# Optimization experiments

Hardware: AMD Instinct MI355X
Metric: run time of the kernel (lower is better)

The kernel has to match this reference:

```python
import jax, jax.numpy as jnp
import numpy as np

B, L, D = 2, 2048, 1024
H, DK, DV = 16, 64, 64
EPS = 1e-6


def setup_inputs() -> dict:
    key = jax.random.key(0)
    ks = jax.random.split(key, 7)
    s = 0.02
    return {
        "x": jax.random.normal(ks[0], (B, L, D), dtype=jnp.float32),
        "Wq": jax.random.normal(ks[1], (D, H * DK), dtype=jnp.float32) * s,
        "Wk": jax.random.normal(ks[2], (D, H * DK), dtype=jnp.float32) * s,
        "Wv": jax.random.normal(ks[3], (D, H * DV), dtype=jnp.float32) * s,
        "Wo": jax.random.normal(ks[4], (H * DV, D), dtype=jnp.float32) * s,
        "ln_gamma": jnp.ones((D,), dtype=jnp.float32),
        "ln_beta": jnp.zeros((D,), dtype=jnp.float32),
    }


def reference(x, Wq, Wk, Wv, Wo, ln_gamma, ln_beta):
    temp = jnp.asarray(DK, x.dtype) ** 0.5
    # projections -> [B, H, L, Dh]
    q = (x @ Wq).reshape(B, L, H, DK).transpose(0, 2, 1, 3)
    k = (x @ Wk).reshape(B, L, H, DK).transpose(0, 2, 1, 3)
    v = (x @ Wv).reshape(B, L, H, DV).transpose(0, 2, 1, 3)
    # naive attention: explicit [B,H,L,L] scores (dropout rate 0 -> identity)
    scores = jnp.einsum("bhqd,bhkd->bhqk", q / temp, k)
    attn = jax.nn.softmax(scores, axis=-1)
    o = jnp.einsum("bhqk,bhkd->bhqd", attn, v)
    o = o.transpose(0, 2, 1, 3).reshape(B, L, H * DV)
    out = o @ Wo + x  # residual
    # LayerNorm(eps=1e-6)
    mu = jnp.mean(out, axis=-1, keepdims=True)
    var = jnp.var(out, axis=-1, keepdims=True)
    return (out - mu) * jax.lax.rsqrt(var + EPS) * ln_gamma + ln_beta
```

## Files before the change

kernel.cpp:

```cpp
#include <hip/hip_runtime.h>


typedef __bf16 bf16;
typedef __bf16 bf16x2 __attribute__((ext_vector_type(2)));
typedef __bf16 bf16x4 __attribute__((ext_vector_type(4)));
typedef __bf16 bf16x8 __attribute__((ext_vector_type(8)));
typedef float floatx4 __attribute__((ext_vector_type(4)));
typedef int intx4 __attribute__((ext_vector_type(4)));

#define MFMA16(a, b, c) __builtin_amdgcn_mfma_f32_16x16x32_bf16((a), (b), (c), 0, 0, 0)

__device__ __forceinline__ void gll16(const bf16* g, bf16* l) {
  __builtin_amdgcn_global_load_lds((const __attribute__((address_space(1))) void*)g,
                                   (__attribute__((address_space(3))) void*)l, 16, 0, 0);
}

__global__ __launch_bounds__(256) void k_prep_x(const float* __restrict__ x, bf16* __restrict__ xb) {
  const int i = (blockIdx.x * 256 + threadIdx.x) * 4;
  const float4 v = *reinterpret_cast<const float4*>(x + i);
  bf16x4 o = {(bf16)v.x, (bf16)v.y, (bf16)v.z, (bf16)v.w};
  *reinterpret_cast<bf16x4*>(xb + i) = o;
}

__global__ __launch_bounds__(256) void k_prep_w(const float* __restrict__ Wq, const float* __restrict__ Wk,
                                                const float* __restrict__ Wv, const float* __restrict__ Wo,
                                                bf16* __restrict__ WT) {
  __shared__ float tile[32][33];
  const int z = blockIdx.z;
  const float* W = (z == 0) ? Wq : (z == 1) ? Wk : (z == 2) ? Wv : Wo;
  const int n0 = blockIdx.x * 32, k0 = blockIdx.y * 32;
  const int tx = threadIdx.x, ty = threadIdx.y;
#pragma unroll
  for (int j = 0; j < 32; j += 8)
    tile[ty + j][tx] = W[(size_t)(k0 + ty + j) * 1024 + n0 + tx];
  __syncthreads();
#pragma unroll
  for (int j = 0; j < 32; j += 8)
    WT[(size_t)(z * 1024 + n0 + ty + j) * 1024 + k0 + tx] = (bf16)tile[tx][ty + j];
}

template <int MODE>
__global__ __launch_bounds__(256) void k_gemm(const bf16* __restrict__ A, const bf16* __restrict__ Bt,
                                              const float* __restrict__ X, float* __restrict__ Y,
                                              bf16* __restrict__ QB, bf16* __restrict__ KB,
                                              bf16* __restrict__ VTB) {
  __shared__ __align__(16) bf16 As[3 * 128 * 64];
  __shared__ __align__(16) bf16 Bs[3 * 128 * 64];
  const int t = threadIdx.x;
  const int lane = t & 63, wv = t >> 6;
  const int qd = lane >> 4, col = lane & 15;
  const int c7 = col & 7;
  const int wm = wv >> 1, wn = wv & 1;
  const int m0 = blockIdx.x * 128, n0 = blockIdx.y * 128;
  const int srow = wv * 8 + (lane >> 3);
  const int scol = ((lane & 7) ^ (lane >> 3)) * 8;
  const bf16* Ag = A + (size_t)(m0 + srow) * 1024 + scol;
  const bf16* Bg = Bt + (size_t)(n0 + srow) * 1024 + scol;

  floatx4 acc[4][4] = {};

#define GSTAGE(bu, ti)                                                                              \
  do {                                                                                              \
    _Pragma("unroll") for (int rd = 0; rd < 4; rd++) {                                              \
      gll16(Ag + (size_t)rd * 32 * 1024 + (ti) * 64, As + (bu) * 8192 + (rd * 32 + wv * 8) * 64);   \
      gll16(Bg + (size_t)rd * 32 * 1024 + (ti) * 64, Bs + (bu) * 8192 + (rd * 32 + wv * 8) * 64);   \
    }                                                                                               \
  } while (0)

#define GCOMP(bu)                                                                                   \
  do {                                                                                              \
    const bf16* as_ = As + (bu) * 8192;                                                             \
    const bf16* bs_ = Bs + (bu) * 8192;                                                             \
    _Pragma("unroll") for (int ks = 0; ks < 2; ks++) {                                              \
      bf16x8 af[4], bfr[4];                                                                         \
      _Pragma("unroll") for (int i = 0; i < 4; i++)                                                 \
        af[i] = *reinterpret_cast<const bf16x8*>(as_ + (wm * 64 + i * 16 + col) * 64 +              \
                                                 ((ks * 4 + qd) ^ c7) * 8);                         \
      _Pragma("unroll") for (int i = 0; i < 4; i++)                                                 \
        bfr[i] = *reinterpret_cast<const bf16x8*>(bs_ + (wn * 64 + i * 16 + col) * 64 +             \
                                                  ((ks * 4 + qd) ^ c7) * 8);                        \
      _Pragma("unroll") for (int i = 0; i < 4; i++)                                                 \
        _Pragma("unroll") for (int j = 0; j < 4; j++)                                               \
          acc[i][j] = MFMA16(af[i], bfr[j], acc[i][j]);                                             \
    }                                                                                               \
  } while (0)

#define GITER(cur, prv, ti)                                            \
  do {                                                                 \
    asm volatile("s_waitcnt vmcnt(8)" ::: "memory");                   \
    __builtin_amdgcn_s_barrier();                                      \
    GCOMP(cur);                                                        \
    __builtin_amdgcn_s_barrier();                                      \
    GSTAGE(prv, ((ti) + 2 <= 15) ? ((ti) + 2) : 15);                   \
  } while (0)

  GSTAGE(0, 0);
  GSTAGE(1, 1);
  asm volatile("s_waitcnt vmcnt(8)" ::: "memory");
  __builtin_amdgcn_s_barrier();
  GCOMP(0);
  __builtin_amdgcn_s_barrier();
  GSTAGE(2, 2);
  for (int j = 1; j < 16; j += 3) {
    GITER(1, 0, j);
    GITER(2, 1, j + 1);
    GITER(0, 2, j + 2);
  }
#undef GSTAGE
#undef GCOMP
#undef GITER

#pragma unroll
  for (int i = 0; i < 4; i++) {
#pragma unroll
    for (int j = 0; j < 4; j++) {
      const int mb = m0 + wm * 64 + i * 16 + qd * 4;
      const int n = n0 + wn * 64 + j * 16 + col;
      if (MODE == 0) {
        const int seg = n >> 10;
        const int h = (n & 1023) >> 6, dd = n & 63;
#pragma unroll
        for (int r = 0; r < 4; r++) {
          const int m = mb + r;
          const int bb = m >> 11, l = m & 2047;
          const float v = acc[i][j][r];
          if (seg == 0)
            QB[((size_t)(bb * 16 + h) * 2048 + l) * 64 + dd] = (bf16)(v * 0.18033688f);
          else if (seg == 1)
            KB[((size_t)(bb * 16 + h) * 2048 + l) * 64 + dd] = (bf16)v;
          else
            VTB[((size_t)(bb * 16 + h) * 64 + dd) * 2048 + l] = (bf16)v;
        }
      } else {
#pragma unroll
        for (int r = 0; r < 4; r++) {
          const int m = mb + r;
          Y[(size_t)m * 1024 + n] = acc[i][j][r] + X[(size_t)m * 1024 + n];
        }
      }
    }
  }
}

__global__ __launch_bounds__(256) void k_attn(const bf16* __restrict__ QB, const bf16* __restrict__ KB,
                                              const bf16* __restrict__ VTB, bf16* __restrict__ OB) {
  __shared__ __align__(16) bf16 Ks[3][64 * 64];
  __shared__ __align__(16) bf16 Vs[3][64 * 64];
  const int t = threadIdx.x;
  const int lane = t & 63, wv = t >> 6;
  const int qd = lane >> 4, col = lane & 15;
  const int c7 = col & 7;
  const int bh = blockIdx.y;
  const int qr = blockIdx.x * 128 + wv * 32;
  const int lrow0 = wv * 8 + (lane >> 3);
  const int scol = ((lane & 7) ^ (lane >> 3)) * 8;
  const int kg0 = ((lrow0 >> 5) << 5) + (((lrow0 >> 2) & 3) << 3) + (((lrow0 >> 4) & 1) << 2) + (lrow0 & 3);
  const int r1 = lrow0 + 32;
  const int kg1 = ((r1 >> 5) << 5) + (((r1 >> 2) & 3) << 3) + (((r1 >> 4) & 1) << 2) + (r1 & 3);
  const bf16* Kg0 = KB + ((size_t)bh * 2048 + kg0) * 64 + scol;
  const bf16* Kg1 = KB + ((size_t)bh * 2048 + kg1) * 64 + scol;
  const bf16* Vg0 = VTB + ((size_t)bh * 64 + lrow0) * 2048 + scol;
  const bf16* Vg1 = VTB + ((size_t)bh * 64 + lrow0 + 32) * 2048 + scol;

  bf16x8 bQ[2][2];
#pragma unroll
  for (int qt = 0; qt < 2; qt++)
#pragma unroll
    for (int s = 0; s < 2; s++)
      bQ[qt][s] = *reinterpret_cast<const bf16x8*>(QB + ((size_t)bh * 2048 + qr + qt * 16 + col) * 64 + s * 32 + qd * 8);

  floatx4 oacc[2][4] = {};
  float lsum[2] = {0.f, 0.f};
  floatx4 scur[2][4];
  int pk[2][4][2];

#define STAGE(bu, ti)                                                  \
  do {                                                                 \
    gll16(Kg0 + (size_t)(ti) * 4096, &Ks[bu][(wv * 8) * 64]);          \
    gll16(Kg1 + (size_t)(ti) * 4096, &Ks[bu][(32 + wv * 8) * 64]);     \
    gll16(Vg0 + (ti) * 64, &Vs[bu][(wv * 8) * 64]);                    \
    gll16(Vg1 + (ti) * 64, &Vs[bu][(32 + wv * 8) * 64]);               \
  } while (0)

#define QK(bu)                                                                                      \
  do {                                                                                              \
    const bf16* ks_ = Ks[bu];                                                                       \
    _Pragma("unroll") for (int nt = 0; nt < 4; nt++) {                                              \
      bf16x8 a0 = *reinterpret_cast<const bf16x8*>(ks_ + (nt * 16 + col) * 64 + (qd ^ c7) * 8);     \
      bf16x8 a1 = *reinterpret_cast<const bf16x8*>(ks_ + (nt * 16 + col) * 64 + ((4 + qd) ^ c7) * 8); \
      _Pragma("unroll") for (int qt = 0; qt < 2; qt++) {                                            \
        floatx4 zz = {0.f, 0.f, 0.f, 0.f};                                                          \
        zz = MFMA16(a0, bQ[qt][0], zz);                                                             \
        zz = MFMA16(a1, bQ[qt][1], zz);                                                             \
        scur[qt][nt] = zz;                                                                          \
      }                                                                                             \
    }                                                                                               \
  } while (0)

#define EXPPACK()                                                                               \
  do {                                                                                          \
    _Pragma("unroll") for (int qt = 0; qt < 2; qt++) {                                          \
      _Pragma("unroll") for (int nt = 0; nt < 4; nt++) {                                        \
        const float e0 = __builtin_amdgcn_exp2f(scur[qt][nt][0]);                               \
        const float e1 = __builtin_amdgcn_exp2f(scur[qt][nt][1]);                               \
        const float e2 = __builtin_amdgcn_exp2f(scur[qt][nt][2]);                               \
        const float e3 = __builtin_amdgcn_exp2f(scur[qt][nt][3]);                               \
        lsum[qt] += (e0 + e1) + (e2 + e3);                                                      \
        bf16x2 p01, p23;                                                                        \
        p01[0] = (bf16)e0; p01[1] = (bf16)e1;                                                   \
        p23[0] = (bf16)e2; p23[1] = (bf16)e3;                                                   \
        pk[qt][nt][0] = __builtin_bit_cast(int, p01);                                           \
        pk[qt][nt][1] = __builtin_bit_cast(int, p23);                                           \
      }                                                                                         \
    }                                                                                           \
  } while (0)

#define PV(bu)                                                                                      \
  do {                                                                                              \
    const bf16* vs_ = Vs[bu];                                                                       \
    bf16x8 bV[4][2];                                                                                \
    _Pragma("unroll") for (int nd = 0; nd < 4; nd++) {                                              \
      bV[nd][0] = *reinterpret_cast<const bf16x8*>(vs_ + (nd * 16 + col) * 64 + (qd ^ c7) * 8);     \
      bV[nd][1] = *reinterpret_cast<const bf16x8*>(vs_ + (nd * 16 + col) * 64 + ((4 + qd) ^ c7) * 8); \
    }                                                                                               \
    _Pragma("unroll") for (int qt = 0; qt < 2; qt++) {                                              \
      _Pragma("unroll") for (int s = 0; s < 2; s++) {                                               \
        intx4 w;                                                                                    \
        w[0] = pk[qt][2 * s][0]; w[1] = pk[qt][2 * s][1];                                           \
        w[2] = pk[qt][2 * s + 1][0]; w[3] = pk[qt][2 * s + 1][1];                                   \
        const bf16x8 aP = __builtin_bit_cast(bf16x8, w);                                            \
        _Pragma("unroll") for (int nd = 0; nd < 4; nd++)                                            \
          oacc[qt][nd] = MFMA16(aP, bV[nd][s], oacc[qt][nd]);                                       \
      }                                                                                             \
    }                                                                                               \
  } while (0)

#define ITER(cur, prv, ti)                                             \
  do {                                                                 \
    asm volatile("s_waitcnt vmcnt(4)" ::: "memory");                   \
    __builtin_amdgcn_s_barrier();                                      \
    EXPPACK();                                                         \
    QK(cur);                                                           \
    PV(prv);                                                           \
    __builtin_amdgcn_s_barrier();                                      \
    STAGE(prv, ((ti) + 2 <= 31) ? ((ti) + 2) : 31);                    \
  } while (0)

  STAGE(0, 0);
  STAGE(1, 1);
  asm volatile("s_waitcnt vmcnt(4)" ::: "memory");
  __builtin_amdgcn_s_barrier();
  QK(0);
  __builtin_amdgcn_s_barrier();
  STAGE(2, 2);
  for (int j = 1; j < 30; j += 3) {
    ITER(1, 0, j);
    ITER(2, 1, j + 1);
    ITER(0, 2, j + 2);
  }
  ITER(1, 0, 31);
  EXPPACK();
  PV(1);

#pragma unroll
  for (int qt = 0; qt < 2; qt++) {
    lsum[qt] += __shfl_xor(lsum[qt], 16);
    lsum[qt] += __shfl_xor(lsum[qt], 32);
  }
  const int bb = bh >> 4, h = bh & 15;
#pragma unroll
  for (int qt = 0; qt < 2; qt++) {
#pragma unroll
    for (int r = 0; r < 4; r++) {
      const float linv = 1.f / __shfl(lsum[qt], qd * 4 + r);
      const size_t m = (size_t)bb * 2048 + qr + qt * 16 + qd * 4 + r;
#pragma unroll
      for (int nd = 0; nd < 4; nd++)
        OB[m * 1024 + h * 64 + nd * 16 + col] = (bf16)(oacc[qt][nd][r] * linv);
    }
  }
#undef STAGE
#undef QK
#undef EXPPACK
#undef PV
#undef ITER
}

__global__ __launch_bounds__(256) void k_ln(const float* __restrict__ Yin, const float* __restrict__ gamma,
                                            const float* __restrict__ beta, float* __restrict__ out) {
  __shared__ float red[8];
  const int row = blockIdx.x, t = threadIdx.x;
  const float4 v = *reinterpret_cast<const float4*>(Yin + (size_t)row * 1024 + t * 4);
  float s = v.x + v.y + v.z + v.w;
  float ss = v.x * v.x + v.y * v.y + v.z * v.z + v.w * v.w;
#pragma unroll
  for (int d = 1; d < 64; d <<= 1) {
    s += __shfl_xor(s, d);
    ss += __shfl_xor(ss, d);
  }
  if ((t & 63) == 0) {
    red[t >> 6] = s;
    red[4 + (t >> 6)] = ss;
  }
  __syncthreads();
  s = red[0] + red[1] + red[2] + red[3];
  ss = red[4] + red[5] + red[6] + red[7];
  const float mu = s * (1.f / 1024.f);
  const float var = ss * (1.f / 1024.f) - mu * mu;
  const float rs = rsqrtf(var + 1e-6f);
  const float4 g = *reinterpret_cast<const float4*>(gamma + t * 4);
  const float4 bt = *reinterpret_cast<const float4*>(beta + t * 4);
  float4 o;
  o.x = (v.x - mu) * rs * g.x + bt.x;
  o.y = (v.y - mu) * rs * g.y + bt.y;
  o.z = (v.z - mu) * rs * g.z + bt.z;
  o.w = (v.w - mu) * rs * g.w + bt.w;
  *reinterpret_cast<float4*>(out + (size_t)row * 1024 + t * 4) = o;
}

extern "C" void kernel_launch(void* const* d_in, const int* in_sizes, int n_in,
                              void* d_out, int out_size, void* d_ws, size_t ws_size,
                              hipStream_t stream) {
  (void)in_sizes; (void)n_in; (void)out_size; (void)ws_size;
  const float* x = (const float*)d_in[0];
  const float* Wq = (const float*)d_in[1];
  const float* Wk = (const float*)d_in[2];
  const float* Wv = (const float*)d_in[3];
  const float* Wo = (const float*)d_in[4];
  const float* gamma = (const float*)d_in[5];
  const float* beta = (const float*)d_in[6];

  char* ws = (char*)d_ws;
  const size_t MB = 1ull << 20;
  bf16* XB = (bf16*)(ws);
  bf16* OB = (bf16*)(ws);
  bf16* WT = (bf16*)(ws + 8 * MB);
  bf16* QB = (bf16*)(ws + 16 * MB);
  bf16* KB = (bf16*)(ws + 24 * MB);
  bf16* VTB = (bf16*)(ws + 32 * MB);
  float* Y = (float*)(ws + 16 * MB);

  k_prep_x<<<4096, 256, 0, stream>>>(x, XB);
  k_prep_w<<<dim3(32, 32, 4), dim3(32, 8), 0, stream>>>(Wq, Wk, Wv, Wo, WT);
  k_gemm<0><<<dim3(32, 24), 256, 0, stream>>>(XB, WT, nullptr, nullptr, QB, KB, VTB);
  k_attn<<<dim3(16, 32), 256, 0, stream>>>(QB, KB, VTB, OB);
  k_gemm<1><<<dim3(32, 8), 256, 0, stream>>>(OB, WT + (size_t)3072 * 1024, x, Y,
                                             nullptr, nullptr, nullptr);
  k_ln<<<4096, 256, 0, stream>>>(Y, gamma, beta, (float*)d_out);
}
```

Before: 210.1 us.

## Use 256x256 tiled QKV GEMM and double-buffer the generic GEMM

Adds a new 512-thread QKV projection kernel with 256x256 output tiles, each wave computing 128x64, and a double-buffered async LDS pipeline. The larger tile raises arithmetic intensity and cuts global reloads of A and B. The trade is 192 blocks on a large GPU, which means lower occupancy and under one wave of blocks per CU. The output-projection GEMM also moves from a triple-buffered pipeline with partial vmcnt waits to double buffering with full vmcnt(0) waits and __syncthreads. That exposes more memory latency in that kernel.

```diff
diff --git a/kernel.cpp b/kernel.cpp
--- a/kernel.cpp
+++ b/kernel.cpp
@@ -39,13 +39,104 @@
     WT[(size_t)(z * 1024 + n0 + ty + j) * 1024 + k0 + tx] = (bf16)tile[tx][ty + j];
 }
 
+__global__ __launch_bounds__(512) void k_gemm256(const bf16* __restrict__ A, const bf16* __restrict__ Bt,
+                                                 bf16* __restrict__ QB, bf16* __restrict__ KB,
+                                                 bf16* __restrict__ VTB) {
+  __shared__ __align__(16) bf16 As[2 * 256 * 64];
+  __shared__ __align__(16) bf16 Bs[2 * 256 * 64];
+  const int t = threadIdx.x;
+  const int lane = t & 63, wv = t >> 6;
+  const int qd = lane >> 4, col = lane & 15;
+  const int c7 = col & 7;
+  const int wm = wv >> 2, wn = wv & 3;
+  const int m0 = blockIdx.x * 256, n0 = blockIdx.y * 256;
+  const int srow = wv * 8 + (lane >> 3);
+  const int scol = ((lane & 7) ^ (lane >> 3)) * 8;
+  const bf16* Ag = A + (size_t)(m0 + srow) * 1024 + scol;
+  const bf16* Bg = Bt + (size_t)(n0 + srow) * 1024 + scol;
+
+  floatx4 acc[8][4] = {};
+
+#define GSTAGE(bu, ti)                                                                               \
+  do {                                                                                               \
+    _Pragma("unroll") for (int rd = 0; rd < 4; rd++) {                                               \
+      gll16(Ag + (size_t)rd * 64 * 1024 + (ti) * 64, As + (bu) * 16384 + (rd * 64 + wv * 8) * 64);   \
+      gll16(Bg + (size_t)rd * 64 * 1024 + (ti) * 64, Bs + (bu) * 16384 + (rd * 64 + wv * 8) * 64);   \
+    }                                                                                                \
+  } while (0)
+
+#define GCOMP(bu)                                                                                    \
+  do {                                                                                               \
+    const bf16* as_ = As + (bu) * 16384;                                                             \
+    const bf16* bs_ = Bs + (bu) * 16384;                                                             \
+    _Pragma("unroll") for (int ks = 0; ks < 2; ks++) {                                               \
+      bf16x8 af[8], bfr[4];                                                                          \
+      _Pragma("unroll") for (int i = 0; i < 8; i++)                                                  \
+        af[i] = *reinterpret_cast<const bf16x8*>(as_ + (wm * 128 + i * 16 + col) * 64 +              \
+                                                 ((ks * 4 + qd) ^ c7) * 8);                          \
+      _Pragma("unroll") for (int j = 0; j < 4; j++)                                                  \
+        bfr[j] = *reinterpret_cast<const bf16x8*>(bs_ + (wn * 64 + j * 16 + col) * 64 +              \
+                                                  ((ks * 4 + qd) ^ c7) * 8);                         \
+      _Pragma("unroll") for (int i = 0; i < 8; i++)                                                  \
+        _Pragma("unroll") for (int j = 0; j < 4; j++)                                                \
+          acc[i][j] = MFMA16(af[i], bfr[j], acc[i][j]);                                              \
+    }                                                                                                \
+  } while (0)
+
+  GSTAGE(0, 0);
+  GSTAGE(1, 1);
+  for (int ti = 0; ti < 14; ti += 2) {
+    asm volatile("s_waitcnt vmcnt(8)" ::: "memory");
+    __builtin_amdgcn_s_barrier();
+    GCOMP(0);
+    __builtin_amdgcn_s_barrier();
+    GSTAGE(0, ti + 2);
+    asm volatile("s_waitcnt vmcnt(8)" ::: "memory");
+    __builtin_amdgcn_s_barrier();
+    GCOMP(1);
+    __builtin_amdgcn_s_barrier();
+    GSTAGE(1, ti + 3);
+  }
+  asm volatile("s_waitcnt vmcnt(8)" ::: "memory");
+  __builtin_amdgcn_s_barrier();
+  GCOMP(0);
+  asm volatile("s_waitcnt vmcnt(0)" ::: "memory");
+  __builtin_amdgcn_s_barrier();
+  GCOMP(1);
+#undef GSTAGE
+#undef GCOMP
+
+#pragma unroll
+  for (int i = 0; i < 8; i++) {
+#pragma unroll
+    for (int j = 0; j < 4; j++) {
+      const int mb = m0 + wm * 128 + i * 16 + qd * 4;
+      const int n = n0 + wn * 64 + j * 16 + col;
+      const int seg = n >> 10;
+      const int h = (n & 1023) >> 6, dd = n & 63;
+#pragma unroll
+      for (int r = 0; r < 4; r++) {
+        const int m = mb + r;
+        const int bb = m >> 11, l = m & 2047;
+        const float v = acc[i][j][r];
+        if (seg == 0)
+          QB[((size_t)(bb * 16 + h) * 2048 + l) * 64 + dd] = (bf16)(v * 0.18033688f);
+        else if (seg == 1)
+          KB[((size_t)(bb * 16 + h) * 2048 + l) * 64 + dd] = (bf16)v;
+        else
+          VTB[((size_t)(bb * 16 + h) * 64 + dd) * 2048 + l] = (bf16)v;
+      }
+    }
+  }
+}
+
 template <int MODE>
 __global__ __launch_bounds__(256) void k_gemm(const bf16* __restrict__ A, const bf16* __restrict__ Bt,
                                               const float* __restrict__ X, float* __restrict__ Y,
                                               bf16* __restrict__ QB, bf16* __restrict__ KB,
                                               bf16* __restrict__ VTB) {
-  __shared__ __align__(16) bf16 As[3 * 128 * 64];
-  __shared__ __align__(16) bf16 Bs[3 * 128 * 64];
+  __shared__ __align__(16) bf16 As[2 * 128 * 64];
+  __shared__ __align__(16) bf16 Bs[2 * 128 * 64];
   const int t = threadIdx.x;
   const int lane = t & 63, wv = t >> 6;
   const int qd = lane >> 4, col = lane & 15;
@@ -59,18 +150,18 @@
 
   floatx4 acc[4][4] = {};
 
-#define GSTAGE(bu, ti)                                                                              \
+#define GSTAGE(ktv, buf)                                                                            \
   do {                                                                                              \
     _Pragma("unroll") for (int rd = 0; rd < 4; rd++) {                                              \
-      gll16(Ag + (size_t)rd * 32 * 1024 + (ti) * 64, As + (bu) * 8192 + (rd * 32 + wv * 8) * 64);   \
-      gll16(Bg + (size_t)rd * 32 * 1024 + (ti) * 64, Bs + (bu) * 8192 + (rd * 32 + wv * 8) * 64);   \
+      gll16(Ag + (size_t)rd * 32 * 1024 + (ktv), As + (buf) * 8192 + (rd * 32 + wv * 8) * 64);      \
+      gll16(Bg + (size_t)rd * 32 * 1024 + (ktv), Bs + (buf) * 8192 + (rd * 32 + wv * 8) * 64);      \
     }                                                                                               \
   } while (0)
 
-#define GCOMP(bu)                                                                                   \
+#define GCOMP(buf)                                                                                  \
   do {                                                                                              \
-    const bf16* as_ = As + (bu) * 8192;                                                             \
-    const bf16* bs_ = Bs + (bu) * 8192;                                                             \
+    const bf16* as_ = As + (buf) * 8192;                                                            \
+    const bf16* bs_ = Bs + (buf) * 8192;                                                            \
     _Pragma("unroll") for (int ks = 0; ks < 2; ks++) {                                              \
       bf16x8 af[4], bfr[4];                                                                         \
       _Pragma("unroll") for (int i = 0; i < 4; i++)                                                 \
@@ -85,30 +176,22 @@
     }                                                                                               \
   } while (0)
 
-#define GITER(cur, prv, ti)                                            \
-  do {                                                                 \
-    asm volatile("s_waitcnt vmcnt(8)" ::: "memory");                   \
-    __builtin_amdgcn_s_barrier();                                      \
-    GCOMP(cur);                                                        \
-    __builtin_amdgcn_s_barrier();                                      \
-    GSTAGE(prv, ((ti) + 2 <= 15) ? ((ti) + 2) : 15);                   \
-  } while (0)
-
   GSTAGE(0, 0);
-  GSTAGE(1, 1);
-  asm volatile("s_waitcnt vmcnt(8)" ::: "memory");
-  __builtin_amdgcn_s_barrier();
-  GCOMP(0);
-  __builtin_amdgcn_s_barrier();
-  GSTAGE(2, 2);
-  for (int j = 1; j < 16; j += 3) {
-    GITER(1, 0, j);
-    GITER(2, 1, j + 1);
-    GITER(0, 2, j + 2);
+  asm volatile("s_waitcnt vmcnt(0)" ::: "memory");
+  __syncthreads();
+
+  for (int kt = 0; kt < 1024; kt += 128) {
+    GSTAGE(kt + 64, 1);
+    GCOMP(0);
+    asm volatile("s_waitcnt vmcnt(0)" ::: "memory");
+    __syncthreads();
+    if (kt + 128 < 1024) GSTAGE(kt + 128, 0);
+    GCOMP(1);
+    asm volatile("s_waitcnt vmcnt(0)" ::: "memory");
+    __syncthreads();
   }
 #undef GSTAGE
 #undef GCOMP
-#undef GITER
 
 #pragma unroll
   for (int i = 0; i < 4; i++) {
@@ -342,7 +425,7 @@
 
   k_prep_x<<<4096, 256, 0, stream>>>(x, XB);
   k_prep_w<<<dim3(32, 32, 4), dim3(32, 8), 0, stream>>>(Wq, Wk, Wv, Wo, WT);
-  k_gemm<0><<<dim3(32, 24), 256, 0, stream>>>(XB, WT, nullptr, nullptr, QB, KB, VTB);
+  k_gemm256<<<dim3(16, 12), 512, 0, stream>>>(XB, WT, QB, KB, VTB);
   k_attn<<<dim3(16, 32), 256, 0, stream>>>(QB, KB, VTB, OB);
   k_gemm<1><<<dim3(32, 8), 256, 0, stream>>>(OB, WT + (size_t)3072 * 1024, x, Y,
                                              nullptr, nullptr, nullptr);
```

Result: slower. 216.4 us (+3.0%).
